# Kernel tuning notes

Measured on AMD Instinct MI355X. Metric: run time of the kernel, lower is better.

## Reference

```python
import jax, jax.numpy as jnp
import numpy as np

N = 4096
IN_CH = 256
OUT_CH = 256
NUM_REL = 8


def setup_inputs() -> dict:
    key = jax.random.key(0)
    k_x, k_a, k_e, k_w = jax.random.split(key, 4)
    x = jax.random.normal(k_x, (N, IN_CH), dtype=jnp.float32)
    A = jax.random.uniform(k_a, (N, N), dtype=jnp.float32)
    edge_type = jax.random.randint(k_e, (N, N), 0, NUM_REL, dtype=jnp.int32)
    # xavier_uniform per-relation weight [R, in, out]
    limit = np.sqrt(6.0 / (IN_CH + OUT_CH))
    weight = jax.random.uniform(k_w, (NUM_REL, IN_CH, OUT_CH), dtype=jnp.float32,
                                minval=-limit, maxval=limit)
    bias = jnp.zeros((OUT_CH,), dtype=jnp.float32)
    return {"x": x, "A": A, "edge_type": edge_type, "weight": weight, "bias": bias}


def reference(x, A, edge_type, weight, bias):
    # out = sum_r ((A * [edge_type == r]) @ x) @ W_r + bias
    num_rel = weight.shape[0]
    out = jnp.zeros((x.shape[0], weight.shape[2]), dtype=x.dtype)
    for rel in range(num_rel):  # small fixed relation count
        rel_adj = A * (edge_type == rel).astype(x.dtype)   # [N, N]
        h = rel_adj @ x                                     # [N, in]
        out = out + h @ weight[rel]                         # [N, out]
    out = out + bias
    return out
```

## Files before the change

### kernel.cpp

```cpp
#include <hip/hip_runtime.h>
#include <stdint.h>


#define NN 4096

typedef __attribute__((ext_vector_type(8)))  short s16x8;
typedef __attribute__((ext_vector_type(16))) float f32x16;
typedef __attribute__((ext_vector_type(4)))  float fx4;
typedef __attribute__((ext_vector_type(4)))  int   ix4;
typedef __attribute__((ext_vector_type(4)))  unsigned int ux4;

union uq { ux4 u; s16x8 s; };

__device__ __forceinline__ unsigned short f2bf(float f) {
  union { float f; unsigned int u; } v; v.f = f;
  unsigned int r = v.u + 0x7fffu + ((v.u >> 16) & 1u);
  return (unsigned short)(r >> 16);
}

__device__ __forceinline__ void gld16(const void* g, void* l) {
  __builtin_amdgcn_global_load_lds(
      (const __attribute__((address_space(1))) unsigned int*)(uintptr_t)g,
      (__attribute__((address_space(3))) unsigned int*)(uintptr_t)l, 16, 0, 0);
}

__global__ void k_init(const float* __restrict__ bias, float* __restrict__ out) {
  int idx = blockIdx.x * 256 + threadIdx.x;
  out[idx] = bias[idx & 255];
}

__global__ __launch_bounds__(256, 2) void k_y(const float* __restrict__ x,
                                              const float* __restrict__ W,
                                              unsigned short* __restrict__ yt) {
  __shared__ unsigned short Wl[128 * 256];
  const int t  = threadIdx.x;
  const int j0 = blockIdx.x * 128;
  const int o0 = blockIdx.y * 16;

  {
    const int r = t >> 5, kc = t & 31;
#pragma unroll
    for (int u = 0; u < 8; ++u) {
      const int k = kc * 8 + u;
      const fx4* wp = (const fx4*)(W + ((size_t)r * 256 + k) * 256 + o0);
      fx4 w[4] = { wp[0], wp[1], wp[2], wp[3] };
#pragma unroll
      for (int i = 0; i < 16; ++i) {
        const int row = i * 8 + r;
        const int gs  = (k >> 3) ^ (row & 7);
        Wl[row * 256 + gs * 8 + (k & 7)] = f2bf(w[i >> 2][i & 3]);
      }
    }
  }
  __syncthreads();

  const int lane = t & 63, wid = t >> 6;
  const int l15 = lane & 15, lh = lane >> 4;
  const int npb = wid * 32;

  fx4 acc[8][2];
#pragma unroll
  for (int m = 0; m < 8; ++m)
#pragma unroll
    for (int n = 0; n < 2; ++n) acc[m][n] = 0.f;

  unsigned int qb[2];
#pragma unroll
  for (int n = 0; n < 2; ++n) {
    int row = npb + n * 16 + l15;
    qb[n] = (unsigned)(row * 512 + 16 * (lh ^ (row & 3))) ^ (64u * ((row >> 2) & 1));
  }
  const char* WlB = (const char*)Wl;
  const float* xb = x + (size_t)(j0 + l15) * 256 + lh * 8;

#pragma unroll
  for (int ks = 0; ks < 8; ++ks) {
    s16x8 a[8];
#pragma unroll
    for (int m = 0; m < 8; ++m) {
      const fx4* xp = (const fx4*)(xb + (size_t)m * 16 * 256 + ks * 32);
      fx4 x0 = xp[0], x1 = xp[1];
      s16x8 av;
#pragma unroll
      for (int i = 0; i < 4; ++i) av[i] = (short)f2bf(x0[i]);
#pragma unroll
      for (int i = 0; i < 4; ++i) av[4 + i] = (short)f2bf(x1[i]);
      a[m] = av;
    }
#pragma unroll
    for (int n = 0; n < 2; ++n) {
      s16x8 b = *(const s16x8*)(WlB + (qb[n] ^ (unsigned)(ks * 64)));
#pragma unroll
      for (int m = 0; m < 8; ++m)
        acc[m][n] = __builtin_amdgcn_mfma_f32_16x16x32_bf16(a[m], b, acc[m][n], 0, 0, 0);
    }
  }

#pragma unroll
  for (int m = 0; m < 8; ++m)
#pragma unroll
    for (int n = 0; n < 2; ++n)
#pragma unroll
      for (int q = 0; q < 4; ++q) {
        int jl = m * 16 + lh * 4 + q;
        int np = npb + n * 16 + l15;
        int o  = o0 + (np >> 3);
        yt[((size_t)(j0 + jl) * 256 + o) * 8 + (np & 7)] = f2bf(acc[m][n][q]);
      }
}

__global__ __launch_bounds__(512, 2) void k_main(const float* __restrict__ A,
                                                 const int*   __restrict__ et,
                                                 const unsigned short* __restrict__ yt,
                                                 float* __restrict__ dst,
                                                 int usePart) {
  __shared__ ux4 smem[9216];
  char* smc = (char*)smem;
  const int t = threadIdx.x, lane = t & 63, w = t >> 6;
  const int l31 = lane & 31, lh1 = lane >> 5;
  const int wm = w & 3, wn = w >> 2;
  const int i0 = blockIdx.x * 256;
  const int kz = blockIdx.y;
  const int jb = kz * 256;

  const int di = t >> 1, dq = t & 1;
  const int lq = dq ^ ((di >> 2) & 1);
  const float* srcA = A  + (size_t)(i0 + di) * NN + jb + lq * 4;
  const int*   srcE = et + (size_t)(i0 + di) * NN + jb + lq * 4;
  const ux4* ytg = (const ux4*)yt;
  const size_t bsrc0 = (size_t)jb * 256 + w * 256 + lane;

#define ISSUE(sq, pbase) do {                                             \
    gld16(srcA + (size_t)(sq) * 8, smc + (pbase) + w * 1024);             \
    gld16(srcE + (size_t)(sq) * 8, smc + (pbase) + 8192 + w * 1024);      \
    _Pragma("unroll")                                                     \
    for (int u = 0; u < 4; ++u)                                           \
      gld16(ytg + bsrc0 + (size_t)(sq) * 2048 + u * 64,                   \
            smc + (pbase) + 16384 + w * 4096 + u * 1024);                 \
  } while (0)

  unsigned rA[2];
#pragma unroll
  for (int m = 0; m < 2; ++m) {
    int il = wm * 64 + m * 32 + l31;
    rA[m] = (unsigned)(il * 32 + ((lh1 ^ ((il >> 2) & 1)) << 4));
  }
  unsigned rB[4];
#pragma unroll
  for (int n = 0; n < 4; ++n)
    rB[n] = (unsigned)(16384 + lh1 * 16384 + (wn * 128 + n * 32 + l31) * 16);

  f32x16 acc[2][4];
#pragma unroll
  for (int m = 0; m < 2; ++m)
#pragma unroll
    for (int n = 0; n < 4; ++n) acc[m][n] = 0.f;

  ISSUE(0, 0);
  ISSUE(1, 49152);

  int pb0 = 0, pb1 = 49152, pb2 = 98304;
  for (int s = 0; s < 32; ++s) {
    asm volatile("s_waitcnt vmcnt(6)" ::: "memory");
    __builtin_amdgcn_s_barrier();
    {
      const int sq = (s + 2 < 32) ? s + 2 : 31;
      ISSUE(sq, pb2);
    }
    fx4 av[2]; ix4 ev[2];
#pragma unroll
    for (int m = 0; m < 2; ++m) {
      av[m] = *(const fx4*)(smc + pb0 + rA[m]);
      ev[m] = *(const ix4*)(smc + pb0 + 8192 + rA[m]);
    }
#pragma unroll
    for (int ks = 0; ks < 4; ++ks) {
      uq a[2];
#pragma unroll
      for (int m = 0; m < 2; ++m) {
        float avv = av[m][ks]; int evv = ev[m][ks];
        unsigned long long sh = ((unsigned long long)f2bf(avv)) << ((evv & 3) * 16);
        unsigned lo = (unsigned)sh, hi = (unsigned)(sh >> 32);
        bool c = evv < 4;
        ux4 q; q.x = c ? lo : 0u; q.y = c ? hi : 0u; q.z = c ? 0u : lo; q.w = c ? 0u : hi;
        a[m].u = q;
      }
#pragma unroll
      for (int n = 0; n < 4; ++n) {
        uq b; b.u = *(const ux4*)(smc + pb0 + rB[n] + (unsigned)(ks * 4096));
#pragma unroll
        for (int m = 0; m < 2; ++m)
          acc[m][n] = __builtin_amdgcn_mfma_f32_32x32x16_bf16(a[m].s, b.s, acc[m][n], 0, 0, 0);
      }
    }
    int tmp = pb0; pb0 = pb1; pb1 = pb2; pb2 = tmp;
  }
  asm volatile("s_waitcnt vmcnt(0)" ::: "memory");

  if (usePart) {
    float* pp = dst + ((size_t)kz << 20);
#pragma unroll
    for (int m = 0; m < 2; ++m)
#pragma unroll
      for (int n = 0; n < 4; ++n)
#pragma unroll
        for (int q = 0; q < 16; ++q) {
          int gi = i0 + wm * 64 + m * 32 + (q & 3) + 8 * (q >> 2) + 4 * lh1;
          int go = wn * 128 + n * 32 + l31;
          pp[(size_t)gi * 256 + go] = acc[m][n][q];
        }
  } else {
#pragma unroll
    for (int m = 0; m < 2; ++m)
#pragma unroll
      for (int n = 0; n < 4; ++n)
#pragma unroll
        for (int q = 0; q < 16; ++q) {
          int gi = i0 + wm * 64 + m * 32 + (q & 3) + 8 * (q >> 2) + 4 * lh1;
          int go = wn * 128 + n * 32 + l31;
          atomicAdd(dst + (size_t)gi * 256 + go, acc[m][n][q]);
        }
  }
#undef ISSUE
}

__global__ __launch_bounds__(256) void k_red(const float* __restrict__ part,
                                             const float* __restrict__ bias,
                                             float* __restrict__ out) {
  int idx = blockIdx.x * 256 + threadIdx.x;
  fx4 s = *(const fx4*)(bias + ((idx << 2) & 255));
  const fx4* p4 = (const fx4*)part;
#pragma unroll
  for (int k = 0; k < 16; ++k) s += p4[((size_t)k << 18) + idx];
  ((fx4*)out)[idx] = s;
}

extern "C" void kernel_launch(void* const* d_in, const int* in_sizes, int n_in,
                              void* d_out, int out_size, void* d_ws, size_t ws_size,
                              hipStream_t stream) {
  const float* x    = (const float*)d_in[0];
  const float* A    = (const float*)d_in[1];
  const int*   et   = (const int*)d_in[2];
  const float* W    = (const float*)d_in[3];
  const float* bias = (const float*)d_in[4];
  float* out = (float*)d_out;
  unsigned short* yt = (unsigned short*)d_ws;

  const size_t YT = (size_t)16 << 20;
  const bool usePart = ws_size >= YT + ((size_t)64 << 20);

  k_y<<<dim3(32, 16), dim3(256), 0, stream>>>(x, W, yt);
  if (usePart) {
    float* pbuf = (float*)((char*)d_ws + YT);
    k_main<<<dim3(16, 16), dim3(512), 0, stream>>>(A, et, yt, pbuf, 1);
    k_red<<<dim3(1024), dim3(256), 0, stream>>>(pbuf, bias, out);
  } else {
    k_init<<<dim3(4096), dim3(256), 0, stream>>>(bias, out);
    k_main<<<dim3(16, 16), dim3(512), 0, stream>>>(A, et, yt, out, 0);
  }
}
```

Measured before the change: 127.9 us.

## Shrink main GEMM tile to 128x128 with output-column split and smaller pipeline stages

Re-tiles the main kernel from 256-row x 256-col blocks of 512 threads to 128x128 blocks of 256 threads, adding an output-column grid dimension and halving the per-stage K depth (64 stages of 4 columns). A and edge_type are now loaded with 4-byte global-to-LDS copies instead of 16-byte ones, and LDS per block drops sharply to allow more resident blocks. It also raises wave priority around the MFMA section. The cost is that A and edge_type are read twice (once per output half), the global loads are narrower, and there are more barrier iterations.

```diff
diff --git a/kernel.cpp b/kernel.cpp
--- a/kernel.cpp
+++ b/kernel.cpp
@@ -22,6 +22,11 @@
   __builtin_amdgcn_global_load_lds(
       (const __attribute__((address_space(1))) unsigned int*)(uintptr_t)g,
       (__attribute__((address_space(3))) unsigned int*)(uintptr_t)l, 16, 0, 0);
+}
+__device__ __forceinline__ void gld4(const void* g, void* l) {
+  __builtin_amdgcn_global_load_lds(
+      (const __attribute__((address_space(1))) unsigned int*)(uintptr_t)g,
+      (__attribute__((address_space(3))) unsigned int*)(uintptr_t)l, 4, 0, 0);
 }
 
 __global__ void k_init(const float* __restrict__ bias, float* __restrict__ out) {
@@ -109,76 +114,89 @@
       }
 }
 
-__global__ __launch_bounds__(512, 2) void k_main(const float* __restrict__ A,
+__global__ __launch_bounds__(256, 4) void k_main(const float* __restrict__ A,
                                                  const int*   __restrict__ et,
                                                  const unsigned short* __restrict__ yt,
                                                  float* __restrict__ dst,
                                                  int usePart) {
-  __shared__ ux4 smem[9216];
+  __shared__ ux4 smem[2304];
   char* smc = (char*)smem;
   const int t = threadIdx.x, lane = t & 63, w = t >> 6;
   const int l31 = lane & 31, lh1 = lane >> 5;
-  const int wm = w & 3, wn = w >> 2;
-  const int i0 = blockIdx.x * 256;
-  const int kz = blockIdx.y;
+  const int wm = w >> 1, wn = w & 1;
+  const int i0 = blockIdx.x * 128;
+  const int o0 = blockIdx.y * 128;
+  const int kz = blockIdx.z;
   const int jb = kz * 256;
 
-  const int di = t >> 1, dq = t & 1;
-  const int lq = dq ^ ((di >> 2) & 1);
-  const float* srcA = A  + (size_t)(i0 + di) * NN + jb + lq * 4;
-  const int*   srcE = et + (size_t)(i0 + di) * NN + jb + lq * 4;
+  const float* srcA[2]; const int* srcE[2];
+#pragma unroll
+  for (int u = 0; u < 2; ++u) {
+    int elem = u * 256 + t;
+    size_t off = (size_t)(i0 + (elem >> 2)) * NN + jb + (elem & 3);
+    srcA[u] = A + off; srcE[u] = et + off;
+  }
   const ux4* ytg = (const ux4*)yt;
-  const size_t bsrc0 = (size_t)jb * 256 + w * 256 + lane;
-
-#define ISSUE(sq, pbase) do {                                             \
-    gld16(srcA + (size_t)(sq) * 8, smc + (pbase) + w * 1024);             \
-    gld16(srcE + (size_t)(sq) * 8, smc + (pbase) + 8192 + w * 1024);      \
-    _Pragma("unroll")                                                     \
-    for (int u = 0; u < 4; ++u)                                           \
-      gld16(ytg + bsrc0 + (size_t)(sq) * 2048 + u * 64,                   \
-            smc + (pbase) + 16384 + w * 4096 + u * 1024);                 \
+  const ux4* srcB[2];
+#pragma unroll
+  for (int u = 0; u < 2; ++u)
+    srcB[u] = ytg + ((size_t)jb + u * 2 + (t >> 7)) * 256 + o0 + (t & 127);
+
+#define ISSUE(sq, pbase) do {                                              \
+    _Pragma("unroll")                                                      \
+    for (int u = 0; u < 2; ++u)                                            \
+      gld4(srcA[u] + (size_t)(sq) * 4, smc + (pbase) + u * 1024 + w * 256);\
+    _Pragma("unroll")                                                      \
+    for (int u = 0; u < 2; ++u)                                            \
+      gld4(srcE[u] + (size_t)(sq) * 4,                                     \
+           smc + (pbase) + 2048 + u * 1024 + w * 256);                     \
+    _Pragma("unroll")                                                      \
+    for (int u = 0; u < 2; ++u)                                            \
+      gld16(srcB[u] + (size_t)(sq) * 1024,                                 \
+            smc + (pbase) + 4096 + u * 4096 + w * 1024);                   \
   } while (0)
 
-  unsigned rA[2];
-#pragma unroll
-  for (int m = 0; m < 2; ++m) {
-    int il = wm * 64 + m * 32 + l31;
-    rA[m] = (unsigned)(il * 32 + ((lh1 ^ ((il >> 2) & 1)) << 4));
-  }
-  unsigned rB[4];
-#pragma unroll
-  for (int n = 0; n < 4; ++n)
-    rB[n] = (unsigned)(16384 + lh1 * 16384 + (wn * 128 + n * 32 + l31) * 16);
-
-  f32x16 acc[2][4];
+  unsigned rA[2], rB[2][2];
 #pragma unroll
   for (int m = 0; m < 2; ++m)
-#pragma unroll
-    for (int n = 0; n < 4; ++n) acc[m][n] = 0.f;
+    rA[m] = (unsigned)((wm * 64 + m * 32 + l31) * 16);
+#pragma unroll
+  for (int ks = 0; ks < 2; ++ks)
+#pragma unroll
+    for (int n = 0; n < 2; ++n)
+      rB[ks][n] = (unsigned)(4096 + ((ks * 2 + lh1) * 128 + wn * 64 + n * 32 + l31) * 16);
+
+  f32x16 acc[2][2];
+#pragma unroll
+  for (int m = 0; m < 2; ++m)
+#pragma unroll
+    for (int n = 0; n < 2; ++n) acc[m][n] = 0.f;
 
   ISSUE(0, 0);
-  ISSUE(1, 49152);
-
-  int pb0 = 0, pb1 = 49152, pb2 = 98304;
-  for (int s = 0; s < 32; ++s) {
+  ISSUE(1, 12288);
+
+  int pb0 = 0, pb1 = 12288, pb2 = 24576;
+  for (int s = 0; s < 64; ++s) {
     asm volatile("s_waitcnt vmcnt(6)" ::: "memory");
     __builtin_amdgcn_s_barrier();
     {
-      const int sq = (s + 2 < 32) ? s + 2 : 31;
+      const int sq = (s + 2 < 64) ? s + 2 : 63;
       ISSUE(sq, pb2);
     }
     fx4 av[2]; ix4 ev[2];
 #pragma unroll
     for (int m = 0; m < 2; ++m) {
       av[m] = *(const fx4*)(smc + pb0 + rA[m]);
-      ev[m] = *(const ix4*)(smc + pb0 + 8192 + rA[m]);
-    }
-#pragma unroll
-    for (int ks = 0; ks < 4; ++ks) {
-      uq a[2];
+      ev[m] = *(const ix4*)(smc + pb0 + 2048 + rA[m]);
+    }
+    __builtin_amdgcn_s_setprio(1);
+#pragma unroll
+    for (int ks = 0; ks < 2; ++ks) {
+      uq a[2], b[2];
 #pragma unroll
       for (int m = 0; m < 2; ++m) {
-        float avv = av[m][ks]; int evv = ev[m][ks];
+        float avv = lh1 ? av[m][ks * 2 + 1] : av[m][ks * 2];
+        int   evv = lh1 ? ev[m][ks * 2 + 1] : ev[m][ks * 2];
         unsigned long long sh = ((unsigned long long)f2bf(avv)) << ((evv & 3) * 16);
         unsigned lo = (unsigned)sh, hi = (unsigned)(sh >> 32);
         bool c = evv < 4;
@@ -186,13 +204,15 @@
         a[m].u = q;
       }
 #pragma unroll
-      for (int n = 0; n < 4; ++n) {
-        uq b; b.u = *(const ux4*)(smc + pb0 + rB[n] + (unsigned)(ks * 4096));
-#pragma unroll
-        for (int m = 0; m < 2; ++m)
-          acc[m][n] = __builtin_amdgcn_mfma_f32_32x32x16_bf16(a[m].s, b.s, acc[m][n], 0, 0, 0);
-      }
-    }
+      for (int n = 0; n < 2; ++n)
+        b[n].u = *(const ux4*)(smc + pb0 + rB[ks][n]);
+#pragma unroll
+      for (int m = 0; m < 2; ++m)
+#pragma unroll
+        for (int n = 0; n < 2; ++n)
+          acc[m][n] = __builtin_amdgcn_mfma_f32_32x32x16_bf16(a[m].s, b[n].s, acc[m][n], 0, 0, 0);
+    }
+    __builtin_amdgcn_s_setprio(0);
     int tmp = pb0; pb0 = pb1; pb1 = pb2; pb2 = tmp;
   }
   asm volatile("s_waitcnt vmcnt(0)" ::: "memory");
@@ -202,22 +222,22 @@
 #pragma unroll
     for (int m = 0; m < 2; ++m)
 #pragma unroll
-      for (int n = 0; n < 4; ++n)
+      for (int n = 0; n < 2; ++n)
 #pragma unroll
         for (int q = 0; q < 16; ++q) {
           int gi = i0 + wm * 64 + m * 32 + (q & 3) + 8 * (q >> 2) + 4 * lh1;
-          int go = wn * 128 + n * 32 + l31;
+          int go = o0 + wn * 64 + n * 32 + l31;
           pp[(size_t)gi * 256 + go] = acc[m][n][q];
         }
   } else {
 #pragma unroll
     for (int m = 0; m < 2; ++m)
 #pragma unroll
-      for (int n = 0; n < 4; ++n)
+      for (int n = 0; n < 2; ++n)
 #pragma unroll
         for (int q = 0; q < 16; ++q) {
           int gi = i0 + wm * 64 + m * 32 + (q & 3) + 8 * (q >> 2) + 4 * lh1;
-          int go = wn * 128 + n * 32 + l31;
+          int go = o0 + wn * 64 + n * 32 + l31;
           atomicAdd(dst + (size_t)gi * 256 + go, acc[m][n][q]);
         }
   }
@@ -252,10 +272,10 @@
   k_y<<<dim3(32, 16), dim3(256), 0, stream>>>(x, W, yt);
   if (usePart) {
     float* pbuf = (float*)((char*)d_ws + YT);
-    k_main<<<dim3(16, 16), dim3(512), 0, stream>>>(A, et, yt, pbuf, 1);
+    k_main<<<dim3(32, 2, 16), dim3(256), 0, stream>>>(A, et, yt, pbuf, 1);
     k_red<<<dim3(1024), dim3(256), 0, stream>>>(pbuf, bias, out);
   } else {
     k_init<<<dim3(4096), dim3(256), 0, stream>>>(bias, out);
-    k_main<<<dim3(16, 16), dim3(512), 0, stream>>>(A, et, yt, out, 0);
-  }
-}
+    k_main<<<dim3(32, 2, 16), dim3(256), 0, stream>>>(A, et, yt, out, 0);
+  }
+}
```

After: 180.5 us. 1.41x slower.
